# Performance work log

Measured on AMD Instinct MI355X. Metric: run time of the kernel, lower is better.

The kernel has to match this reference:

```python
import jax, jax.numpy as jnp
import numpy as np

TOPK = 50
TEMPERATURE = 0.07

def _l2norm(x, eps=1e-12):
    # matches torch F.normalize: x / max(||x||, eps)
    n = jnp.sqrt(jnp.sum(x * x, axis=-1, keepdims=True))
    return x / jnp.clip(n, eps)

def setup_inputs() -> dict:
    key = jax.random.key(0)
    ks = jax.random.split(key, 16)
    B, D, C, M, V = 1024, 128, 256, 100000, 100000
    s = 1.0 / np.sqrt(D)
    s2 = 1.0 / np.sqrt(2 * D)
    sc = 1.0 / np.sqrt(C)
    return {
        "current_repr": jax.random.normal(ks[0], (B, D), jnp.float32),
        "session_ids": jax.random.randint(ks[1], (B,), 0, V),
        "item_emb": jax.random.normal(ks[2], (V, D), jnp.float32),
        "feature_queue": jax.random.normal(ks[3], (M, D), jnp.float32),
        "session_queue": jax.random.randint(ks[4], (M,), 0, V),
        "target_queue": jax.random.randint(ks[5], (M,), 0, V),
        "Wq": jax.random.normal(ks[6], (D, D), jnp.float32) * s,
        "bq": jnp.zeros((D,), jnp.float32),
        "Wk": jax.random.normal(ks[7], (D, D), jnp.float32) * s,
        "bk": jnp.zeros((D,), jnp.float32),
        "W1": jax.random.normal(ks[8], (2 * D, C), jnp.float32) * s2,
        "b1": jnp.zeros((C,), jnp.float32),
        "W2": jax.random.normal(ks[9], (C, C), jnp.float32) * sc,
        "b2": jnp.zeros((C,), jnp.float32),
        "fallback_context": jnp.zeros((D,), jnp.float32),
        "fallback_summary": jnp.zeros((C,), jnp.float32),
    }

def reference(current_repr, session_ids, item_emb, feature_queue, session_queue,
              target_queue, Wq, bq, Wk, bk, W1, b1, W2, b2,
              fallback_context, fallback_summary):
    # cosine similarity between projected queries and projected bank keys
    q = _l2norm(current_repr @ Wq + bq)            # [B, D]
    k = _l2norm(feature_queue @ Wk + bk)           # [M, D]
    sims = q @ k.T                                  # [B, M]
    # mask entries from the same session
    valid = session_queue[None, :] != session_ids[:, None]
    sims = jnp.where(valid, sims, -jnp.inf)
    top_values, top_idx = jax.lax.top_k(sims, TOPK)  # [B, K]
    sel = jnp.isfinite(top_values)
    used = jnp.any(sel, axis=1)                      # [B]
    logits = jnp.where(sel, top_values / TEMPERATURE, -1e9)
    attn = jax.nn.softmax(logits, axis=1) * sel.astype(logits.dtype)
    attn = attn / jnp.clip(jnp.sum(attn, axis=1, keepdims=True), 1e-12)
    nbr_feat = feature_queue[top_idx]                # [B, K, D]
    nbr_tgt = jnp.clip(target_queue[top_idx], 0)     # [B, K]
    context = jnp.einsum('bk,bkd->bd', attn, nbr_feat)
    tgt_emb = item_emb[nbr_tgt]                      # [B, K, D]
    h = jnp.concatenate([nbr_feat, tgt_emb], axis=-1)  # [B, K, 2D]
    h = jax.nn.gelu(h @ W1 + b1, approximate=False) @ W2 + b2  # [B, K, C]
    summary = jnp.einsum('bk,bkd->bd', attn, h)
    context = jnp.where(used[:, None], context, fallback_context[None, :])
    summary = jnp.where(used[:, None], summary, fallback_summary[None, :])
    return context, summary, used
```

## Files before the change

kernel.cpp:

```cpp
#include <hip/hip_runtime.h>
#include <hip/hip_bf16.h>

#define TOPK 50
#define CAP 512
#define MQ 100000
#define ZCUT 2.9f
#define EPS2 0.006f
#define NS_BLK 49
#define NS_CNT 12500.0f
#define NAPP ((MQ + 255) / 256)

typedef float f32x4 __attribute__((ext_vector_type(4)));
typedef __bf16 bf16x8 __attribute__((ext_vector_type(8)));
typedef unsigned short u16x8 __attribute__((ext_vector_type(8)));
typedef unsigned short u16x4 __attribute__((ext_vector_type(4)));

__device__ __forceinline__ unsigned short f2bf(float f) {
    unsigned int u = __float_as_uint(f);
    return (unsigned short)((u + 0x7fffu + ((u >> 16) & 1u)) >> 16);
}
__device__ __forceinline__ float bf2f(unsigned short u) {
    return __uint_as_float(((unsigned int)u) << 16);
}

__global__ void k_transpose(const float* __restrict__ W1, const float* __restrict__ W2,
                            unsigned short* __restrict__ W1t, unsigned short* __restrict__ W2t) {
    int c = blockIdx.x & 255;
    int k = threadIdx.x;
    if (blockIdx.x < 256) W1t[c*256 + k] = f2bf(W1[k*256 + c]);
    else                  W2t[c*256 + k] = f2bf(W2[k*256 + c]);
}

__global__ void k_qproj(const float* __restrict__ cr, const float* __restrict__ Wq,
                        const float* __restrict__ bq,
                        double* __restrict__ q64, unsigned short* __restrict__ qbf) {
    int row = blockIdx.x, d = threadIdx.x;
    __shared__ double xs[128];
    __shared__ double red[128];
    xs[d] = (double)cr[row*128 + d];
    __syncthreads();
    double s = (double)bq[d];
    #pragma unroll 4
    for (int i = 0; i < 128; ++i) s += xs[i] * (double)Wq[i*128 + d];
    red[d] = s * s;
    __syncthreads();
    for (int off = 64; off > 0; off >>= 1) {
        if (d < off) red[d] += red[d + off];
        __syncthreads();
    }
    double inv = 1.0 / fmax(sqrt(red[0]), 1e-12);
    double qv = s * inv;
    q64[row*128 + d] = qv;
    qbf[row*128 + d] = f2bf((float)qv);
}

__global__ __launch_bounds__(256) void k_kproj(const float* __restrict__ fq,
        const float* __restrict__ Wk, const float* __restrict__ bk,
        unsigned short* __restrict__ k_hi, double* __restrict__ invn) {
    __shared__ __align__(16) float wks[128*128];
    __shared__ __align__(16) float fqs[128*129];
    int t = threadIdx.x;
    long row0 = (long)blockIdx.x * 128;
    for (int j = 0; j < 16; ++j) {
        int id4 = t + 256*j;
        float4 v = reinterpret_cast<const float4*>(Wk)[id4];
        *reinterpret_cast<float4*>(&wks[id4*4]) = v;
    }
    for (int j = 0; j < 16; ++j) {
        int id4 = t + 256*j;
        int r = id4 >> 5;
        int c4 = (id4 & 31) << 2;
        float4 v = {0.f, 0.f, 0.f, 0.f};
        if (row0 + r < MQ) v = *reinterpret_cast<const float4*>(&fq[(row0 + r)*128 + c4]);
        fqs[r*129 + c4 + 0] = v.x;
        fqs[r*129 + c4 + 1] = v.y;
        fqs[r*129 + c4 + 2] = v.z;
        fqs[r*129 + c4 + 3] = v.w;
    }
    __syncthreads();
    const int ct = t & 15, rt = t >> 4;
    const int r0 = rt * 8, c0 = ct * 4;
    float acc[8][8];
    #pragma unroll
    for (int a = 0; a < 8; ++a)
        #pragma unroll
        for (int b = 0; b < 8; ++b) acc[a][b] = 0.f;
    #pragma unroll 2
    for (int i = 0; i < 128; ++i) {
        float4 w0 = *reinterpret_cast<const float4*>(&wks[i*128 + c0]);
        float4 w1 = *reinterpret_cast<const float4*>(&wks[i*128 + 64 + c0]);
        float a[8];
        #pragma unroll
        for (int rr = 0; rr < 8; ++rr) a[rr] = fqs[(r0+rr)*129 + i];
        #pragma unroll
        for (int rr = 0; rr < 8; ++rr) {
            acc[rr][0] = fmaf(a[rr], w0.x, acc[rr][0]);
            acc[rr][1] = fmaf(a[rr], w0.y, acc[rr][1]);
            acc[rr][2] = fmaf(a[rr], w0.z, acc[rr][2]);
            acc[rr][3] = fmaf(a[rr], w0.w, acc[rr][3]);
            acc[rr][4] = fmaf(a[rr], w1.x, acc[rr][4]);
            acc[rr][5] = fmaf(a[rr], w1.y, acc[rr][5]);
            acc[rr][6] = fmaf(a[rr], w1.z, acc[rr][6]);
            acc[rr][7] = fmaf(a[rr], w1.w, acc[rr][7]);
        }
    }
    float bkv[8];
    #pragma unroll
    for (int cc = 0; cc < 4; ++cc) { bkv[cc] = bk[c0+cc]; bkv[4+cc] = bk[64+c0+cc]; }
    #pragma unroll
    for (int rr = 0; rr < 8; ++rr)
        #pragma unroll
        for (int cc = 0; cc < 8; ++cc) acc[rr][cc] += bkv[cc];
    __syncthreads();
    double* npart = reinterpret_cast<double*>(fqs);
    #pragma unroll
    for (int rr = 0; rr < 8; ++rr) {
        double pn = 0.0;
        #pragma unroll
        for (int cc = 0; cc < 8; ++cc) pn += (double)acc[rr][cc] * (double)acc[rr][cc];
        npart[(r0+rr)*16 + ct] = pn;
    }
    __syncthreads();
    double* invd = npart + 128*16;
    if (t < 128) {
        double nn = 0.0;
        for (int k2 = 0; k2 < 16; ++k2) nn += npart[t*16 + k2];
        double iv = 1.0 / fmax(sqrt(nn), 1e-12);
        invd[t] = iv;
        if (row0 + t < MQ) invn[row0 + t] = iv;
    }
    __syncthreads();
    #pragma unroll
    for (int rr = 0; rr < 8; ++rr) {
        long row = row0 + r0 + rr;
        if (row < MQ) {
            float iv = (float)invd[r0 + rr];
            u16x4 o0, o1;
            #pragma unroll
            for (int cc = 0; cc < 4; ++cc) {
                o0[cc] = f2bf(acc[rr][cc] * iv);
                o1[cc] = f2bf(acc[rr][4+cc] * iv);
            }
            *reinterpret_cast<u16x4*>(&k_hi[row*128 + c0]) = o0;
            *reinterpret_cast<u16x4*>(&k_hi[row*128 + 64 + c0]) = o1;
        }
    }
}

__global__ __launch_bounds__(256) void k_stats(const unsigned short* __restrict__ qbf,
        const unsigned short* __restrict__ k_hi, float* __restrict__ ws_s) {
    __shared__ float lds_s[4][1024][2];
    int t = threadIdx.x;
    int n = blockIdx.x;
    int w = t >> 6, l = t & 63;
    int lr = l & 15, lk = l >> 4;
    for (int i = t; i < 4*1024*2; i += 256) ((float*)lds_s)[i] = 0.f;
    bf16x8 bfr[4][4];
    #pragma unroll
    for (int cf = 0; cf < 4; ++cf) {
        long scol = 8L * (n*256 + w*64 + cf*16 + lr);
        #pragma unroll
        for (int kk = 0; kk < 4; ++kk) {
            u16x8 v = {0,0,0,0,0,0,0,0};
            if (scol < MQ) v = *reinterpret_cast<const u16x8*>(&k_hi[scol*128 + kk*32 + lk*8]);
            bfr[cf][kk] = *reinterpret_cast<bf16x8*>(&v);
        }
    }
    __syncthreads();
    for (int rg = 0; rg < 64; ++rg) {
        bf16x8 a[4];
        #pragma unroll
        for (int kk = 0; kk < 4; ++kk)
            a[kk] = *reinterpret_cast<const bf16x8*>(&qbf[(rg*16 + lr)*128 + kk*32 + lk*8]);
        f32x4 acc[4];
        #pragma unroll
        for (int cf = 0; cf < 4; ++cf) {
            acc[cf] = (f32x4){0.f,0.f,0.f,0.f};
            #pragma unroll
            for (int kk = 0; kk < 4; ++kk)
                acc[cf] = __builtin_amdgcn_mfma_f32_16x16x32_bf16(a[kk], bfr[cf][kk], acc[cf], 0, 0, 0);
        }
        #pragma unroll
        for (int i = 0; i < 4; ++i) {
            float s1 = acc[0][i] + acc[1][i] + acc[2][i] + acc[3][i];
            float s2 = acc[0][i]*acc[0][i] + acc[1][i]*acc[1][i]
                     + acc[2][i]*acc[2][i] + acc[3][i]*acc[3][i];
            #pragma unroll
            for (int m = 1; m < 16; m <<= 1) {
                s1 += __shfl_xor(s1, m, 64);
                s2 += __shfl_xor(s2, m, 64);
            }
            if (lr == 0) {
                int row = rg*16 + lk*4 + i;
                lds_s[w][row][0] += s1;
                lds_s[w][row][1] += s2;
            }
        }
    }
    __syncthreads();
    for (int r = t; r < 1024; r += 256) {
        float a = lds_s[0][r][0] + lds_s[1][r][0] + lds_s[2][r][0] + lds_s[3][r][0];
        float b = lds_s[0][r][1] + lds_s[1][r][1] + lds_s[2][r][1] + lds_s[3][r][1];
        ws_s[n*2048 + r*2 + 0] = a;
        ws_s[n*2048 + r*2 + 1] = b;
    }
}

__global__ void k_thresh(const float* __restrict__ ws_s, float* __restrict__ Trow) {
    int r = blockIdx.x * 256 + threadIdx.x;
    if (r >= 1024) return;
    float s1 = 0.f, s2 = 0.f;
    for (int n = 0; n < NS_BLK; ++n) {
        s1 += ws_s[n*2048 + r*2 + 0];
        s2 += ws_s[n*2048 + r*2 + 1];
    }
    float mu = s1 / NS_CNT;
    float var = s2 / NS_CNT - mu*mu;
    float sg = sqrtf(fmaxf(var, 1e-12f));
    Trow[r] = mu + ZCUT * sg;
}

__global__ __launch_bounds__(256) void k_append(const unsigned short* __restrict__ qbf,
        const unsigned short* __restrict__ k_hi, const float* __restrict__ Trow,
        const int* __restrict__ sq, const int* __restrict__ sid,
        int* __restrict__ cnt, int* __restrict__ cnthi, int* __restrict__ cand) {
    int t = threadIdx.x;
    int col0 = blockIdx.x * 256;
    int w = t >> 6, l = t & 63;
    int lr = l & 15, lk = l >> 4;
    bf16x8 bfr[4][4];
    int colg[4];
    #pragma unroll
    for (int cf = 0; cf < 4; ++cf) {
        long c = col0 + w*64 + cf*16 + lr;
        colg[cf] = (int)c;
        #pragma unroll
        for (int kk = 0; kk < 4; ++kk) {
            u16x8 v = {0,0,0,0,0,0,0,0};
            if (c < MQ) v = *reinterpret_cast<const u16x8*>(&k_hi[c*128 + kk*32 + lk*8]);
            bfr[cf][kk] = *reinterpret_cast<bf16x8*>(&v);
        }
    }
    for (int rg = 0; rg < 64; ++rg) {
        bf16x8 a[4];
        #pragma unroll
        for (int kk = 0; kk < 4; ++kk)
            a[kk] = *reinterpret_cast<const bf16x8*>(&qbf[(rg*16 + lr)*128 + kk*32 + lk*8]);
        f32x4 T4 = *reinterpret_cast<const f32x4*>(&Trow[rg*16 + lk*4]);
        float Tmin = fminf(fminf(T4[0], T4[1]), fminf(T4[2], T4[3]));
        f32x4 acc[4];
        #pragma unroll
        for (int cf = 0; cf < 4; ++cf) {
            acc[cf] = (f32x4){0.f,0.f,0.f,0.f};
            #pragma unroll
            for (int kk = 0; kk < 4; ++kk)
                acc[cf] = __builtin_amdgcn_mfma_f32_16x16x32_bf16(a[kk], bfr[cf][kk], acc[cf], 0, 0, 0);
        }
        #pragma unroll
        for (int cf = 0; cf < 4; ++cf) {
            float mx = fmaxf(fmaxf(acc[cf][0], acc[cf][1]), fmaxf(acc[cf][2], acc[cf][3]));
            if (mx >= Tmin && colg[cf] < MQ) {
                #pragma unroll
                for (int i = 0; i < 4; ++i) {
                    float v = acc[cf][i];
                    if (v >= T4[i]) {
                        int r = rg*16 + lk*4 + i;
                        int pos = atomicAdd(&cnt[r], 1);
                        if (pos < CAP) cand[r*CAP + pos] = colg[cf];
                        if (v >= T4[i] + EPS2 && sq[colg[cf]] != sid[r])
                            atomicAdd(&cnthi[r], 1);
                    }
                }
            }
        }
    }
}

__global__ __launch_bounds__(256) void k_fix(const unsigned short* __restrict__ qbf,
        const unsigned short* __restrict__ k_hi,
        const int* __restrict__ sq, const int* __restrict__ sid,
        int* __restrict__ cnt, const int* __restrict__ cnthi, int* __restrict__ cand) {
    int row = blockIdx.x;
    if (cnthi[row] >= TOPK && cnt[row] <= CAP) return;
    __shared__ float qr[128];
    __shared__ int hist[1024];
    __shared__ float Tsh;
    int t = threadIdx.x;
    if (t < 128) qr[t] = bf2f(qbf[row*128 + t]);
    for (int i = t; i < 1024; i += 256) hist[i] = 0;
    __syncthreads();
    int myses = sid[row];
    for (int c = t; c < MQ; c += 256) {
        if (sq[c] == myses) continue;
        const u16x8* kr = reinterpret_cast<const u16x8*>(k_hi + (long)c*128);
        float v = 0.f;
        for (int j = 0; j < 16; ++j) {
            u16x8 kv = kr[j];
            #pragma unroll
            for (int e = 0; e < 8; ++e) v += qr[j*8+e] * bf2f(kv[e]);
        }
        int b = (int)((v + 1.0f) * 512.0f);
        b = b < 0 ? 0 : (b > 1023 ? 1023 : b);
        atomicAdd(&hist[b], 1);
    }
    __syncthreads();
    if (t == 0) {
        int cum = 0; float T = -2.0f;
        for (int b = 1023; b >= 0; --b) {
            cum += hist[b];
            if (cum >= TOPK) { T = (float)b * (1.0f/512.0f) - 1.0f - 0.005f; break; }
        }
        Tsh = T;
        cnt[row] = 0;
    }
    __syncthreads();
    float T = Tsh;
    for (int c = t; c < MQ; c += 256) {
        const u16x8* kr = reinterpret_cast<const u16x8*>(k_hi + (long)c*128);
        float v = 0.f;
        for (int j = 0; j < 16; ++j) {
            u16x8 kv = kr[j];
            #pragma unroll
            for (int e = 0; e < 8; ++e) v += qr[j*8+e] * bf2f(kv[e]);
        }
        if (v >= T) {
            int pos = atomicAdd(&cnt[row], 1);
            if (pos < CAP) cand[row*CAP + pos] = c;
        }
    }
}

__global__ __launch_bounds__(256) void k_select(
        const double* __restrict__ q64, const float* __restrict__ Wk,
        const float* __restrict__ bk, const float* __restrict__ fq,
        const double* __restrict__ invn, const int* __restrict__ sq,
        const int* __restrict__ sid, const int* __restrict__ cnt,
        const int* __restrict__ cand,
        float* __restrict__ attn_g, int* __restrict__ tidx_g, int* __restrict__ used_g,
        float* __restrict__ out_ctx, float* __restrict__ out_used,
        const float* __restrict__ fb_ctx) {
    __shared__ double qs[128];
    __shared__ double wqr[128];
    __shared__ double qb_s;
    __shared__ double vals[CAP];
    __shared__ int cidx[CAP];
    __shared__ double selv[TOPK];
    __shared__ int seli[TOPK];
    __shared__ float attn_s[TOPK];
    __shared__ int used_s;
    int row = blockIdx.x, t = threadIdx.x;
    if (t < 128) qs[t] = q64[row*128 + t];
    __syncthreads();
    if (t < 128) {
        double s = 0.0;
        for (int d = 0; d < 128; ++d) s += (double)Wk[t*128 + d] * qs[d];
        wqr[t] = s;
    }
    if (t == 0) {
        double s = 0.0;
        for (int d = 0; d < 128; ++d) s += qs[d] * (double)bk[d];
        qb_s = s;
    }
    if (t < TOPK) { selv[t] = -1e290; seli[t] = 0; }
    __syncthreads();
    int n = cnt[row]; if (n > CAP) n = CAP;
    int myses = sid[row];
    for (int j = t; j < n; j += 256) {
        int c = cand[row*CAP + j];
        cidx[j] = c;
        double v;
        if (sq[c] == myses) v = -1e300;
        else {
            double s = qb_s;
            const float4* xr4 = reinterpret_cast<const float4*>(fq + (long)c*128);
            for (int i4 = 0; i4 < 32; ++i4) {
                float4 x4 = xr4[i4];
                s += (double)x4.x * wqr[i4*4+0] + (double)x4.y * wqr[i4*4+1]
                   + (double)x4.z * wqr[i4*4+2] + (double)x4.w * wqr[i4*4+3];
            }
            v = s * invn[c];
        }
        vals[j] = v;
    }
    __syncthreads();
    for (int j = t; j < n; j += 256) {
        double v = vals[j]; int ci = cidx[j];
        int rk = 0;
        for (int m2 = 0; m2 < n; ++m2) {
            double vm = vals[m2];
            rk += (vm > v) || (vm == v && cidx[m2] < ci);
        }
        if (rk < TOPK) { selv[rk] = v; seli[rk] = ci; }
    }
    __syncthreads();
    if (t == 0) {
        double vmax = -1.0e308;
        for (int r = 0; r < TOPK; ++r)
            if (selv[r] > -1e250 && selv[r] > vmax) vmax = selv[r];
        float ssum = 0.f;
        for (int r = 0; r < TOPK; ++r) {
            float ev = 0.f;
            if (selv[r] > -1e250) ev = expf((float)((selv[r] - vmax) * (1.0/0.07)));
            attn_s[r] = ev; ssum += ev;
        }
        float invs = (ssum > 0.f) ? 1.0f/ssum : 0.0f;
        for (int r = 0; r < TOPK; ++r) attn_s[r] *= invs;
        used_s = (ssum > 0.f) ? 1 : 0;
        used_g[row] = used_s;
    }
    __syncthreads();
    int used = used_s;
    if (t < TOPK) { attn_g[row*TOPK + t] = attn_s[t]; tidx_g[row*TOPK + t] = seli[t]; }
    if (t < 128) {
        float cacc = 0.f;
        for (int r = 0; r < TOPK; ++r) cacc += attn_s[r] * fq[(long)seli[r]*128 + t];
        out_ctx[row*128 + t] = used ? cacc : fb_ctx[t];
    }
    if (t == 0) out_used[row] = used ? 1.0f : 0.0f;
}

__global__ __launch_bounds__(256) void k_mlp(
        const float* __restrict__ fq, const float* __restrict__ item_emb,
        const int* __restrict__ tq,
        const unsigned short* __restrict__ W1t, const unsigned short* __restrict__ W2t,
        const float* __restrict__ b1, const float* __restrict__ b2,
        const float* __restrict__ attn_g, const int* __restrict__ tidx_g,
        const int* __restrict__ used_g,
        const float* __restrict__ fb_sum, float* __restrict__ out_sum) {
    __shared__ __align__(16) unsigned short xs[64*256];
    __shared__ float attn_s[64];
    __shared__ int tgt_s[64];
    __shared__ int tix_s[64];
    int b = blockIdx.x, t = threadIdx.x;
    if (t < 64) {
        float a = 0.f; int ti = 0;
        if (t < TOPK) { a = attn_g[b*TOPK + t]; ti = tidx_g[b*TOPK + t]; }
        attn_s[t] = a; tix_s[t] = ti;
        int tg = 0;
        if (t < TOPK) { tg = tq[ti]; if (tg < 0) tg = 0; }
        tgt_s[t] = tg;
    }
    __syncthreads();
    for (int j = 0; j < 8; ++j) {
        int chunk = t + 256*j;
        int r = chunk >> 5, s = chunk & 31;
        int sp = s ^ (r & 7);
        u16x8 o = {0,0,0,0,0,0,0,0};
        if (r < TOPK) {
            int c0 = s * 8;
            const float* src = (c0 < 128) ? (fq + (long)tix_s[r]*128 + c0)
                                          : (item_emb + (long)tgt_s[r]*128 + (c0 - 128));
            float4 v0 = *reinterpret_cast<const float4*>(src);
            float4 v1 = *reinterpret_cast<const float4*>(src + 4);
            o[0] = f2bf(v0.x); o[1] = f2bf(v0.y); o[2] = f2bf(v0.z); o[3] = f2bf(v0.w);
            o[4] = f2bf(v1.x); o[5] = f2bf(v1.y); o[6] = f2bf(v1.z); o[7] = f2bf(v1.w);
        }
        *reinterpret_cast<u16x8*>(&xs[(r*32 + sp)*8]) = o;
    }
    __syncthreads();
    int w = t >> 6, l = t & 63, lr = l & 15, lk = l >> 4;
    int wbase = w * 64;
    f32x4 zero4 = {0.f, 0.f, 0.f, 0.f};
    f32x4 acc[4][4];
    #pragma unroll
    for (int rt = 0; rt < 4; ++rt)
        #pragma unroll
        for (int ctl = 0; ctl < 4; ++ctl) acc[rt][ctl] = zero4;
    #pragma unroll
    for (int kk = 0; kk < 8; ++kk) {
        bf16x8 av[4];
        #pragma unroll
        for (int rt = 0; rt < 4; ++rt) {
            int r = rt*16 + lr;
            int sp = (kk*4 + lk) ^ (r & 7);
            av[rt] = *reinterpret_cast<const bf16x8*>(&xs[(r*32 + sp)*8]);
        }
        #pragma unroll
        for (int ctl = 0; ctl < 4; ++ctl) {
            int col = wbase + ctl*16 + lr;
            bf16x8 bv = *reinterpret_cast<const bf16x8*>(&W1t[(long)col*256 + kk*32 + lk*8]);
            #pragma unroll
            for (int rt = 0; rt < 4; ++rt)
                acc[rt][ctl] = __builtin_amdgcn_mfma_f32_16x16x32_bf16(av[rt], bv, acc[rt][ctl], 0, 0, 0);
        }
    }
    __syncthreads();
    #pragma unroll
    for (int ctl = 0; ctl < 4; ++ctl) {
        int col = wbase + ctl*16 + lr;
        float b1v = b1[col];
        #pragma unroll
        for (int rt = 0; rt < 4; ++rt) {
            #pragma unroll
            for (int i = 0; i < 4; ++i) {
                int r = rt*16 + lk*4 + i;
                float v = acc[rt][ctl][i] + b1v;
                float g = 0.5f * v * (1.0f + erff(v * 0.70710678118654752f));
                int cchunk = (col >> 3) ^ (r & 7);
                xs[(r*32 + cchunk)*8 + (col & 7)] = f2bf(g);
            }
        }
    }
    __syncthreads();
    f32x4 acc2[4][4];
    #pragma unroll
    for (int rt = 0; rt < 4; ++rt)
        #pragma unroll
        for (int ctl = 0; ctl < 4; ++ctl) acc2[rt][ctl] = zero4;
    #pragma unroll
    for (int kk = 0; kk < 8; ++kk) {
        bf16x8 av[4];
        #pragma unroll
        for (int rt = 0; rt < 4; ++rt) {
            int r = rt*16 + lr;
            int sp = (kk*4 + lk) ^ (r & 7);
            av[rt] = *reinterpret_cast<const bf16x8*>(&xs[(r*32 + sp)*8]);
        }
        #pragma unroll
        for (int ctl = 0; ctl < 4; ++ctl) {
            int col = wbase + ctl*16 + lr;
            bf16x8 bv = *reinterpret_cast<const bf16x8*>(&W2t[(long)col*256 + kk*32 + lk*8]);
            #pragma unroll
            for (int rt = 0; rt < 4; ++rt)
                acc2[rt][ctl] = __builtin_amdgcn_mfma_f32_16x16x32_bf16(av[rt], bv, acc2[rt][ctl], 0, 0, 0);
        }
    }
    int used = used_g[b];
    #pragma unroll
    for (int ctl = 0; ctl < 4; ++ctl) {
        float ps = 0.f;
        #pragma unroll
        for (int rt = 0; rt < 4; ++rt)
            #pragma unroll
            for (int i = 0; i < 4; ++i)
                ps += attn_s[rt*16 + lk*4 + i] * acc2[rt][ctl][i];
        ps += __shfl_xor(ps, 16, 64);
        ps += __shfl_xor(ps, 32, 64);
        if (l < 16) {
            int col = wbase + ctl*16 + l;
            out_sum[b*256 + col] = used ? (ps + b2[col]) : fb_sum[col];
        }
    }
}

extern "C" void kernel_launch(void* const* d_in, const int* in_sizes, int n_in,
                              void* d_out, int out_size, void* d_ws, size_t ws_size,
                              hipStream_t stream) {
    const float* cr   = (const float*)d_in[0];
    const int*   sid  = (const int*)d_in[1];
    const float* item = (const float*)d_in[2];
    const float* fq   = (const float*)d_in[3];
    const int*   sq   = (const int*)d_in[4];
    const int*   tq   = (const int*)d_in[5];
    const float* Wq   = (const float*)d_in[6];
    const float* bq   = (const float*)d_in[7];
    const float* Wk   = (const float*)d_in[8];
    const float* bk   = (const float*)d_in[9];
    const float* W1   = (const float*)d_in[10];
    const float* b1   = (const float*)d_in[11];
    const float* W2   = (const float*)d_in[12];
    const float* b2   = (const float*)d_in[13];
    const float* fbc  = (const float*)d_in[14];
    const float* fbs  = (const float*)d_in[15];

    float* out_ctx  = (float*)d_out;
    float* out_sum  = out_ctx + 1024*128;
    float* out_used = out_sum + 1024*256;

    char* w = (char*)d_ws;
    unsigned short* k_hi = (unsigned short*)w;  w += (size_t)MQ*128*2;
    double* invn = (double*)w;                  w += (size_t)MQ*8;
    double* q64 = (double*)w;                   w += (size_t)1024*128*8;
    unsigned short* qbf = (unsigned short*)w;   w += (size_t)1024*128*2;
    unsigned short* W1t = (unsigned short*)w;   w += (size_t)256*256*2;
    unsigned short* W2t = (unsigned short*)w;   w += (size_t)256*256*2;
    int* cand = (int*)w;                        w += (size_t)1024*CAP*4;
    int* cnt = (int*)w;                         w += (size_t)1024*4;
    int* cnthi = (int*)w;                       w += (size_t)1024*4;
    float* attn_g = (float*)w;                  w += (size_t)1024*TOPK*4;
    int* tidx_g = (int*)w;                      w += (size_t)1024*TOPK*4;
    int* used_g = (int*)w;                      w += (size_t)1024*4;
    float* ws_s = (float*)w;                    w += (size_t)NS_BLK*2048*4;
    float* Trow = (float*)w;                    w += (size_t)1024*4;

    hipMemsetAsync(cnt, 0, 1024*4, stream);
    hipMemsetAsync(cnthi, 0, 1024*4, stream);
    k_transpose<<<512, 256, 0, stream>>>(W1, W2, W1t, W2t);
    k_qproj<<<1024, 128, 0, stream>>>(cr, Wq, bq, q64, qbf);
    k_kproj<<<(MQ + 127)/128, 256, 0, stream>>>(fq, Wk, bk, k_hi, invn);
    k_stats<<<NS_BLK, 256, 0, stream>>>(qbf, k_hi, ws_s);
    k_thresh<<<4, 256, 0, stream>>>(ws_s, Trow);
    k_append<<<NAPP, 256, 0, stream>>>(qbf, k_hi, Trow, sq, sid, cnt, cnthi, cand);
    k_fix<<<1024, 256, 0, stream>>>(qbf, k_hi, sq, sid, cnt, cnthi, cand);
    k_select<<<1024, 256, 0, stream>>>(q64, Wk, bk, fq, invn, sq, sid, cnt, cand,
                                       attn_g, tidx_g, used_g, out_ctx, out_used, fbc);
    k_mlp<<<1024, 256, 0, stream>>>(fq, item, tq, W1t, W2t, b1, b2,
                                    attn_g, tidx_g, used_g, fbs, out_sum);
}
```

Baseline: 754.1 us.

## Split stats and append kernels over query row chunks and prefetch query fragments

k_stats now launches a second grid dimension of 8 row chunks, so 392 blocks replace 49. Its LDS buffer shrinks to 128 rows per block, and the partial-sum layout and k_thresh indexing change to match. k_append splits its 64 query row groups into 4 chunks across blockIdx.y, which gives four times as many blocks. Both kernels also software-prefetch the next query fragment before running the MFMAs. The aim is to fill an under-occupied GPU, mainly in k_stats, at the cost of reloading each key tile once per row chunk.

```diff
diff --git a/kernel.cpp b/kernel.cpp
--- a/kernel.cpp
+++ b/kernel.cpp
@@ -149,12 +149,13 @@
 
 __global__ __launch_bounds__(256) void k_stats(const unsigned short* __restrict__ qbf,
         const unsigned short* __restrict__ k_hi, float* __restrict__ ws_s) {
-    __shared__ float lds_s[4][1024][2];
+    __shared__ float lds_s[4][128][2];
     int t = threadIdx.x;
     int n = blockIdx.x;
+    int rc = blockIdx.y;
     int w = t >> 6, l = t & 63;
     int lr = l & 15, lk = l >> 4;
-    for (int i = t; i < 4*1024*2; i += 256) ((float*)lds_s)[i] = 0.f;
+    for (int i = t; i < 4*128*2; i += 256) ((float*)lds_s)[i] = 0.f;
     bf16x8 bfr[4][4];
     #pragma unroll
     for (int cf = 0; cf < 4; ++cf) {
@@ -167,11 +168,20 @@
         }
     }
     __syncthreads();
-    for (int rg = 0; rg < 64; ++rg) {
+    int rg0 = rc * 8;
+    bf16x8 a_nxt[4];
+    #pragma unroll
+    for (int kk = 0; kk < 4; ++kk)
+        a_nxt[kk] = *reinterpret_cast<const bf16x8*>(&qbf[(rg0*16 + lr)*128 + kk*32 + lk*8]);
+    for (int j = 0; j < 8; ++j) {
         bf16x8 a[4];
         #pragma unroll
-        for (int kk = 0; kk < 4; ++kk)
-            a[kk] = *reinterpret_cast<const bf16x8*>(&qbf[(rg*16 + lr)*128 + kk*32 + lk*8]);
+        for (int kk = 0; kk < 4; ++kk) a[kk] = a_nxt[kk];
+        if (j < 7) {
+            #pragma unroll
+            for (int kk = 0; kk < 4; ++kk)
+                a_nxt[kk] = *reinterpret_cast<const bf16x8*>(&qbf[((rg0+j+1)*16 + lr)*128 + kk*32 + lk*8]);
+        }
         f32x4 acc[4];
         #pragma unroll
         for (int cf = 0; cf < 4; ++cf) {
@@ -191,28 +201,30 @@
                 s2 += __shfl_xor(s2, m, 64);
             }
             if (lr == 0) {
-                int row = rg*16 + lk*4 + i;
-                lds_s[w][row][0] += s1;
-                lds_s[w][row][1] += s2;
+                int rloc = j*16 + lk*4 + i;
+                lds_s[w][rloc][0] += s1;
+                lds_s[w][rloc][1] += s2;
             }
         }
     }
     __syncthreads();
-    for (int r = t; r < 1024; r += 256) {
+    int p = n*8 + rc;
+    for (int r = t; r < 128; r += 256) {
         float a = lds_s[0][r][0] + lds_s[1][r][0] + lds_s[2][r][0] + lds_s[3][r][0];
         float b = lds_s[0][r][1] + lds_s[1][r][1] + lds_s[2][r][1] + lds_s[3][r][1];
-        ws_s[n*2048 + r*2 + 0] = a;
-        ws_s[n*2048 + r*2 + 1] = b;
+        ws_s[p*256 + r*2 + 0] = a;
+        ws_s[p*256 + r*2 + 1] = b;
     }
 }
 
 __global__ void k_thresh(const float* __restrict__ ws_s, float* __restrict__ Trow) {
     int r = blockIdx.x * 256 + threadIdx.x;
     if (r >= 1024) return;
+    int rc = r >> 7, rl = r & 127;
     float s1 = 0.f, s2 = 0.f;
     for (int n = 0; n < NS_BLK; ++n) {
-        s1 += ws_s[n*2048 + r*2 + 0];
-        s2 += ws_s[n*2048 + r*2 + 1];
+        s1 += ws_s[(n*8 + rc)*256 + rl*2 + 0];
+        s2 += ws_s[(n*8 + rc)*256 + rl*2 + 1];
     }
     float mu = s1 / NS_CNT;
     float var = s2 / NS_CNT - mu*mu;
@@ -226,6 +238,7 @@
         int* __restrict__ cnt, int* __restrict__ cnthi, int* __restrict__ cand) {
     int t = threadIdx.x;
     int col0 = blockIdx.x * 256;
+    int rbase = blockIdx.y * 16;
     int w = t >> 6, l = t & 63;
     int lr = l & 15, lk = l >> 4;
     bf16x8 bfr[4][4];
@@ -241,11 +254,20 @@
             bfr[cf][kk] = *reinterpret_cast<bf16x8*>(&v);
         }
     }
-    for (int rg = 0; rg < 64; ++rg) {
+    bf16x8 a_nxt[4];
+    #pragma unroll
+    for (int kk = 0; kk < 4; ++kk)
+        a_nxt[kk] = *reinterpret_cast<const bf16x8*>(&qbf[(rbase*16 + lr)*128 + kk*32 + lk*8]);
+    for (int j = 0; j < 16; ++j) {
+        int rg = rbase + j;
         bf16x8 a[4];
         #pragma unroll
-        for (int kk = 0; kk < 4; ++kk)
-            a[kk] = *reinterpret_cast<const bf16x8*>(&qbf[(rg*16 + lr)*128 + kk*32 + lk*8]);
+        for (int kk = 0; kk < 4; ++kk) a[kk] = a_nxt[kk];
+        if (j < 15) {
+            #pragma unroll
+            for (int kk = 0; kk < 4; ++kk)
+                a_nxt[kk] = *reinterpret_cast<const bf16x8*>(&qbf[((rg+1)*16 + lr)*128 + kk*32 + lk*8]);
+        }
         f32x4 T4 = *reinterpret_cast<const f32x4*>(&Trow[rg*16 + lk*4]);
         float Tmin = fminf(fminf(T4[0], T4[1]), fminf(T4[2], T4[3]));
         f32x4 acc[4];
@@ -588,9 +610,9 @@
     k_transpose<<<512, 256, 0, stream>>>(W1, W2, W1t, W2t);
     k_qproj<<<1024, 128, 0, stream>>>(cr, Wq, bq, q64, qbf);
     k_kproj<<<(MQ + 127)/128, 256, 0, stream>>>(fq, Wk, bk, k_hi, invn);
-    k_stats<<<NS_BLK, 256, 0, stream>>>(qbf, k_hi, ws_s);
+    k_stats<<<dim3(NS_BLK, 8), 256, 0, stream>>>(qbf, k_hi, ws_s);
     k_thresh<<<4, 256, 0, stream>>>(ws_s, Trow);
-    k_append<<<NAPP, 256, 0, stream>>>(qbf, k_hi, Trow, sq, sid, cnt, cnthi, cand);
+    k_append<<<dim3(NAPP, 4), 256, 0, stream>>>(qbf, k_hi, Trow, sq, sid, cnt, cnthi, cand);
     k_fix<<<1024, 256, 0, stream>>>(qbf, k_hi, sq, sid, cnt, cnthi, cand);
     k_select<<<1024, 256, 0, stream>>>(q64, Wk, bk, fq, invn, sq, sid, cnt, cand,
                                        attn_g, tidx_g, used_g, out_ctx, out_used, fbc);
```

Measured after the change: 733.1 us. 2.8% less time.
